# Optimization experiments

Measured on AMD Instinct MI355X. Metric: run time of the kernel, lower is better.

## Reference

```python
import jax, jax.numpy as jnp
import numpy as np

NUM_HEADS = 4
EPS = 1e-5


def conv1(W, b, z):
    # Conv1d with kernel_size=1 == channel-wise linear: (B, Cin, L) -> (B, Cout, L)
    return jnp.einsum('oi,bil->bol', W, z) + b[None, :, None]


def setup_inputs() -> dict:
    key = jax.random.key(0)
    ks = jax.random.split(key, 16)
    B, D, N = 2, 256, 4096
    s = 0.05
    return {
        'x': jax.random.normal(ks[0], (B, D, N), jnp.float32),
        'source': jax.random.normal(ks[1], (B, D, N), jnp.float32),
        'Wq': jax.random.normal(ks[2], (D, D), jnp.float32) * s,
        'bq': jax.random.normal(ks[3], (D,), jnp.float32) * s,
        'Wk': jax.random.normal(ks[4], (D, D), jnp.float32) * s,
        'bk': jax.random.normal(ks[5], (D,), jnp.float32) * s,
        'Wv': jax.random.normal(ks[6], (D, D), jnp.float32) * s,
        'bv': jax.random.normal(ks[7], (D,), jnp.float32) * s,
        'Wm': jax.random.normal(ks[8], (D, D), jnp.float32) * s,
        'bm': jax.random.normal(ks[9], (D,), jnp.float32) * s,
        'W1': jax.random.normal(ks[10], (2 * D, 2 * D), jnp.float32) * s,
        'b1': jax.random.normal(ks[11], (2 * D,), jnp.float32) * s,
        'W2': jax.random.normal(ks[12], (D, 2 * D), jnp.float32) * s,
        'b2': jax.random.normal(ks[13], (D,), jnp.float32) * s,
    }


def reference(x, source, Wq, bq, Wk, bk, Wv, bv, Wm, bm, W1, b1, W2, b2):
    B, D, N = x.shape
    M = source.shape[2]
    H = NUM_HEADS
    dim = D // H  # per-head dim; torch reshape splits channels as (dim, heads)

    q = conv1(Wq, bq, x).reshape(B, dim, H, N)
    k = conv1(Wk, bk, source).reshape(B, dim, H, M)
    v = conv1(Wv, bv, source).reshape(B, dim, H, M)

    scores = jnp.einsum('bdhn,bdhm->bhnm', q, k) / (dim ** 0.5)
    prob = jax.nn.softmax(scores, axis=-1)
    attn = jnp.einsum('bhnm,bdhm->bdhn', prob, v).reshape(B, D, N)

    message = conv1(Wm, bm, attn)

    h = conv1(W1, b1, jnp.concatenate([x, message], axis=1))
    # InstanceNorm1d (affine=False, biased var over L)
    mu = jnp.mean(h, axis=2, keepdims=True)
    var = jnp.mean((h - mu) ** 2, axis=2, keepdims=True)
    h = jax.nn.relu((h - mu) / jnp.sqrt(var + EPS))
    return conv1(W2, b2, h)
```

## Files before the change

### kernel.cpp

```cpp
#include <hip/hip_runtime.h>
#include <cstdint>
#include <cstddef>


typedef __attribute__((ext_vector_type(8))) short short8;
typedef __attribute__((ext_vector_type(4))) float floatx4;

union U4 { unsigned int u[4]; short8 s; };

__device__ __forceinline__ unsigned short f2bf(float x) {
  union { float f; unsigned int u; } c; c.f = x;
  unsigned int r = c.u + 0x7FFFu + ((c.u >> 16) & 1u);
  return (unsigned short)(r >> 16);
}
__device__ __forceinline__ float bf2f(unsigned short u) {
  union { unsigned int i; float f; } c; c.i = ((unsigned int)u) << 16; return c.f;
}
__device__ __forceinline__ void gload16(const void* g, void* l) {
  __builtin_amdgcn_global_load_lds(
      (const __attribute__((address_space(1))) unsigned int*)g,
      (__attribute__((address_space(3))) unsigned int*)l, 16, 0, 0);
}
__device__ __forceinline__ unsigned int cvtpk(float lo, float hi) {
  unsigned int r;
  asm("v_cvt_pk_bf16_f32 %0, %1, %2" : "=v"(r) : "v"(lo), "v"(hi));
  return r;
}

#define LOG2E_8 0.18033688011112042f

__global__ __launch_bounds__(256) void tx_all(
    const float* __restrict__ x, const float* __restrict__ src,
    unsigned short* __restrict__ xb, unsigned short* __restrict__ sb,
    int C, int N)
{
  __shared__ float tile[32][33];
  const int which = blockIdx.z >> 1, b = blockIdx.z & 1;
  const float* X = which ? src : x;
  unsigned short* Y = which ? sb : xb;
  const int n0 = blockIdx.x * 32, c0 = blockIdx.y * 32;
  const int tc = threadIdx.x & 31, tr = threadIdx.x >> 5;
  #pragma unroll
  for (int i = 0; i < 4; ++i)
    tile[tr + i * 8][tc] = X[((size_t)b * C + c0 + tr + i * 8) * N + n0 + tc];
  __syncthreads();
  #pragma unroll
  for (int i = 0; i < 4; ++i)
    Y[((size_t)b * N + n0 + tr + i * 8) * C + c0 + tc] = f2bf(tile[tc][tr + i * 8]);
}

__global__ __launch_bounds__(256) void wprep(
    const float* __restrict__ Wq, const float* __restrict__ Wk,
    const float* __restrict__ Wv, const float* __restrict__ Wm,
    const float* __restrict__ W1, const float* __restrict__ W2,
    const float* __restrict__ bq, const float* __restrict__ bk,
    const float* __restrict__ bv, const float* __restrict__ bm,
    const float* __restrict__ b1, const float* __restrict__ b2,
    unsigned short* __restrict__ wqkv, unsigned short* __restrict__ wm_,
    unsigned short* __restrict__ w1_, unsigned short* __restrict__ w2_,
    float* __restrict__ biasb)
{
  const int bid = blockIdx.x, t = threadIdx.x;
  if (bid < 768) {
    const int idx = bid * 256 + t;
    const int op = idx >> 8, ip = idx & 255;
    const int grp = op >> 8, oo = op & 255;
    const int o = 4 * (oo & 63) + (oo >> 6);
    const float* W = grp == 0 ? Wq : grp == 1 ? Wk : Wv;
    const float sc = grp == 0 ? LOG2E_8 : 1.f;
    wqkv[idx] = f2bf(W[(size_t)o * 256 + ip] * sc);
  } else if (bid < 1024) {
    const int idx = (bid - 768) * 256 + t;
    const int op = idx >> 8, ip = idx & 255;
    const int i2 = 4 * (ip & 63) + (ip >> 6);
    wm_[idx] = f2bf(Wm[(size_t)op * 256 + i2]);
  } else if (bid < 2048) {
    const int idx = (bid - 1024) * 256 + t;
    w1_[idx] = f2bf(W1[idx]);
  } else if (bid < 2560) {
    const int idx = (bid - 2048) * 256 + t;
    w2_[idx] = f2bf(W2[idx]);
  } else {
    const int z = (bid - 2560) * 256 + t;
    if (z < 256)       biasb[z] = bq[4 * (z & 63) + (z >> 6)] * LOG2E_8;
    else if (z < 512)  { const int y = z - 256; biasb[z] = bk[4 * (y & 63) + (y >> 6)]; }
    else if (z < 768)  { const int y = z - 512; biasb[z] = bv[4 * (y & 63) + (y >> 6)]; }
    else if (z < 1024) biasb[z] = bm[z - 768];
    else if (z < 1536) biasb[z] = b1[z - 1024];
    else if (z < 1792) biasb[z] = b2[z - 1536];
  }
}

__global__ __launch_bounds__(256) void gemm128(
    const unsigned short* __restrict__ Wb, const float* __restrict__ bias,
    const unsigned short* __restrict__ X0, const unsigned short* __restrict__ X1,
    void* __restrict__ O0, void* __restrict__ O1, void* __restrict__ O2,
    int Co, int Ci, int Ci0, int N, int variant)
{
  const int n0 = blockIdx.x * 128;
  const int o0 = blockIdx.y * 128;
  const int b  = blockIdx.z;
  const int t  = threadIdx.x;
  const int w = t >> 6, lane = t & 63, qd = lane >> 4, l = lane & 15;
  const int oh = (w >> 1) * 64, nh = (w & 1) * 64;

  __shared__ unsigned short Wl[128 * 64];
  __shared__ unsigned short Xl[128 * 64];

  floatx4 acc[4][4];
  #pragma unroll
  for (int i = 0; i < 4; ++i)
    #pragma unroll
    for (int j = 0; j < 4; ++j) acc[i][j] = (floatx4){0.f, 0.f, 0.f, 0.f};

  for (int k0 = 0; k0 < Ci; k0 += 64) {
    const unsigned short* Xs; int cb, rl;
    if (variant == 1) { Xs = (o0 < 256) ? X0 : X1; cb = k0; rl = Ci; }
    else if (k0 < Ci0) { Xs = X0; cb = k0; rl = Ci0; }
    else               { Xs = X1; cb = k0 - Ci0; rl = Ci - Ci0; }
    __syncthreads();
    #pragma unroll
    for (int i = 0; i < 4; ++i) {
      const int idx = i * 256 + t;
      const int row = idx >> 3, pg = idx & 7, sg = pg ^ (row & 7);
      gload16(&Wb[(size_t)(o0 + row) * Ci + k0 + sg * 8], &Wl[row * 64 + pg * 8]);
      gload16(&Xs[((size_t)b * N + n0 + row) * rl + cb + sg * 8], &Xl[row * 64 + pg * 8]);
    }
    __syncthreads();

    short8 af[4][2], bf[4][2];
    #pragma unroll
    for (int i = 0; i < 4; ++i) {
      const int ar = oh + 16 * i + l;
      af[i][0] = *(const short8*)&Wl[ar * 64 + ((qd ^ (ar & 7))) * 8];
      af[i][1] = *(const short8*)&Wl[ar * 64 + (((4 + qd) ^ (ar & 7))) * 8];
    }
    #pragma unroll
    for (int j = 0; j < 4; ++j) {
      const int br = nh + 16 * j + l;
      bf[j][0] = *(const short8*)&Xl[br * 64 + ((qd ^ (br & 7))) * 8];
      bf[j][1] = *(const short8*)&Xl[br * 64 + (((4 + qd) ^ (br & 7))) * 8];
    }
    #pragma unroll
    for (int i = 0; i < 4; ++i)
      #pragma unroll
      for (int j = 0; j < 4; ++j) {
        acc[i][j] = __builtin_amdgcn_mfma_f32_16x16x32_bf16(af[i][0], bf[j][0], acc[i][j], 0, 0, 0);
        acc[i][j] = __builtin_amdgcn_mfma_f32_16x16x32_bf16(af[i][1], bf[j][1], acc[i][j], 0, 0, 0);
      }
  }

  const int osec = o0 + oh;
  #pragma unroll
  for (int i = 0; i < 4; ++i) {
    const int o4 = o0 + oh + 16 * i + qd * 4;
    const float4 bi = *(const float4*)&bias[o4];
    #pragma unroll
    for (int j = 0; j < 4; ++j) {
      const int n = n0 + nh + 16 * j + l;
      if (variant == 0) {
        unsigned short* C = (unsigned short*)O0;
        ushort4 pk;
        pk.x = f2bf(acc[i][j][0] + bi.x); pk.y = f2bf(acc[i][j][1] + bi.y);
        pk.z = f2bf(acc[i][j][2] + bi.z); pk.w = f2bf(acc[i][j][3] + bi.w);
        *(ushort4*)&C[((size_t)b * N + n) * Co + o4] = pk;
      } else if (variant == 1) {
        if (osec < 256) {
          unsigned short* C = (unsigned short*)O0;
          ushort4 pk;
          pk.x = f2bf(acc[i][j][0] + bi.x); pk.y = f2bf(acc[i][j][1] + bi.y);
          pk.z = f2bf(acc[i][j][2] + bi.z); pk.w = f2bf(acc[i][j][3] + bi.w);
          *(ushort4*)&C[((size_t)b * N + n) * 256 + o4] = pk;
        } else if (osec < 512) {
          unsigned short* C = (unsigned short*)O1;
          ushort4 pk;
          pk.x = f2bf(acc[i][j][0] + bi.x); pk.y = f2bf(acc[i][j][1] + bi.y);
          pk.z = f2bf(acc[i][j][2] + bi.z); pk.w = f2bf(acc[i][j][3] + bi.w);
          *(ushort4*)&C[((size_t)b * N + n) * 256 + (o4 - 256)] = pk;
        } else {
          unsigned short* C = (unsigned short*)O2;
          #pragma unroll
          for (int rg = 0; rg < 4; ++rg) {
            const int op = o4 - 512 + rg, h = op >> 6, d = op & 63;
            C[(((size_t)b * 4 + h) * 64 + d) * N + n] =
                f2bf(acc[i][j][rg] + ((const float*)&bi)[rg]);
          }
        }
      } else {
        float* C = (float*)O0;
        #pragma unroll
        for (int rg = 0; rg < 4; ++rg)
          C[((size_t)b * Co + o4 + rg) * N + n] = acc[i][j][rg] + ((const float*)&bi)[rg];
      }
    }
  }
}

__global__ __launch_bounds__(256) void attn_mfma(
    const unsigned short* __restrict__ qb, const unsigned short* __restrict__ kb,
    const unsigned short* __restrict__ vh, unsigned short* __restrict__ Opart,
    float* __restrict__ liPart, int N)
{
  const int qt = blockIdx.x;
  const int h  = blockIdx.y;
  const int b  = blockIdx.z >> 2, s = blockIdx.z & 3;
  const int n0 = qt * 128;
  const int t  = threadIdx.x;
  const int w = t >> 6, lane = t & 63, qd = lane >> 4, l = lane & 15;

  __shared__ unsigned short Kl[2][64 * 64];
  __shared__ unsigned short Vl[2][64 * 64];

  const unsigned short* qp0 = &qb[((size_t)b * N + n0 + 16 * w + l) * 256 + h * 64];
  const unsigned short* qp1 = qp0 + (size_t)64 * 256;
  short8 bQ[2][2];
  bQ[0][0] = *(const short8*)&qp0[qd * 8];
  bQ[0][1] = *(const short8*)&qp0[32 + qd * 8];
  bQ[1][0] = *(const short8*)&qp1[qd * 8];
  bQ[1][1] = *(const short8*)&qp1[32 + qd * 8];

  short8 ones;
  #pragma unroll
  for (int i = 0; i < 8; ++i) ones[i] = (short)0x3F80;

  floatx4 accO[2][4];
  floatx4 accLi[2];
  #pragma unroll
  for (int qs = 0; qs < 2; ++qs) {
    accLi[qs] = (floatx4){0.f, 0.f, 0.f, 0.f};
    #pragma unroll
    for (int ds = 0; ds < 4; ++ds) accO[qs][ds] = (floatx4){0.f, 0.f, 0.f, 0.f};
  }

  const int j0base = s * 1024;

  auto STAGE = [&](int buf, int j0) {
    #pragma unroll
    for (int i = 0; i < 2; ++i) {
      const int idx = i * 256 + t;
      const int row = idx >> 3, pg = idx & 7, sg = pg ^ (row & 7);
      gload16(&kb[((size_t)b * N + j0 + row) * 256 + h * 64 + sg * 8],
              &Kl[buf][row * 64 + pg * 8]);
      gload16(&vh[(((size_t)b * 4 + h) * 64 + row) * N + j0 + sg * 8],
              &Vl[buf][row * 64 + pg * 8]);
    }
  };

  STAGE(0, j0base);

  #pragma unroll 2
  for (int jt = 0; jt < 16; ++jt) {
    const int cur = jt & 1;
    __syncthreads();
    if (jt < 15) STAGE(cur ^ 1, j0base + (jt + 1) * 64);

    floatx4 S[2][4];
    __builtin_amdgcn_s_setprio(1);
    #pragma unroll
    for (int js = 0; js < 4; ++js) {
      const int br = 16 * js + l;
      const short8 k0 = *(const short8*)&Kl[cur][br * 64 + ((qd ^ (br & 7))) * 8];
      const short8 k1 = *(const short8*)&Kl[cur][br * 64 + (((4 + qd) ^ (br & 7))) * 8];
      floatx4 a0 = (floatx4){0.f, 0.f, 0.f, 0.f};
      floatx4 a1 = (floatx4){0.f, 0.f, 0.f, 0.f};
      a0 = __builtin_amdgcn_mfma_f32_16x16x32_bf16(k0, bQ[0][0], a0, 0, 0, 0);
      a1 = __builtin_amdgcn_mfma_f32_16x16x32_bf16(k0, bQ[1][0], a1, 0, 0, 0);
      a0 = __builtin_amdgcn_mfma_f32_16x16x32_bf16(k1, bQ[0][1], a0, 0, 0, 0);
      a1 = __builtin_amdgcn_mfma_f32_16x16x32_bf16(k1, bQ[1][1], a1, 0, 0, 0);
      S[0][js] = a0; S[1][js] = a1;
    }
    __builtin_amdgcn_s_setprio(0);

    unsigned int T[2][2][4];
    #pragma unroll
    for (int qs = 0; qs < 2; ++qs) {
      unsigned int U[4], W[4];
      #pragma unroll
      for (int js = 0; js < 4; ++js) {
        const float p0 = __builtin_exp2f(S[qs][js][0]);
        const float p1 = __builtin_exp2f(S[qs][js][1]);
        const float p2 = __builtin_exp2f(S[qs][js][2]);
        const float p3 = __builtin_exp2f(S[qs][js][3]);
        U[js] = cvtpk(p0, p1);
        W[js] = cvtpk(p2, p3);
      }
      #pragma unroll
      for (int js2 = 0; js2 < 2; ++js2) {
        unsigned int t0 = U[2 * js2], t2 = U[2 * js2 + 1];
        asm("v_permlane32_swap_b32 %0, %1" : "+v"(t0), "+v"(t2));
        asm("v_permlane16_swap_b32 %0, %1" : "+v"(t0), "+v"(t2));
        unsigned int t1 = W[2 * js2], t3 = W[2 * js2 + 1];
        asm("v_permlane32_swap_b32 %0, %1" : "+v"(t1), "+v"(t3));
        asm("v_permlane16_swap_b32 %0, %1" : "+v"(t1), "+v"(t3));
        T[qs][js2][0] = t0; T[qs][js2][1] = t1;
        T[qs][js2][2] = t2; T[qs][js2][3] = t3;
      }
    }

    __builtin_amdgcn_s_setprio(1);
    #pragma unroll
    for (int js2 = 0; js2 < 2; ++js2) {
      short8 vv[4];
      #pragma unroll
      for (int ds = 0; ds < 4; ++ds) {
        const int vr = 16 * ds + l;
        vv[ds] = *(const short8*)&Vl[cur][vr * 64 + (((4 * js2 + qd) ^ (vr & 7))) * 8];
      }
      #pragma unroll
      for (int qs = 0; qs < 2; ++qs) {
        U4 pu;
        pu.u[0] = T[qs][js2][0]; pu.u[1] = T[qs][js2][1];
        pu.u[2] = T[qs][js2][2]; pu.u[3] = T[qs][js2][3];
        const short8 pa = pu.s;
        #pragma unroll
        for (int ds = 0; ds < 4; ++ds)
          accO[qs][ds] = __builtin_amdgcn_mfma_f32_16x16x32_bf16(pa, vv[ds], accO[qs][ds], 0, 0, 0);
        accLi[qs] = __builtin_amdgcn_mfma_f32_16x16x32_bf16(pa, ones, accLi[qs], 0, 0, 0);
      }
    }
    __builtin_amdgcn_s_setprio(0);
  }

  const size_t obase = ((((size_t)b * 4 + h) * 4 + s) * 32 + qt) * 128;
  #pragma unroll
  for (int qs = 0; qs < 2; ++qs)
    #pragma unroll
    for (int rg = 0; rg < 4; ++rg) {
      const int q = qs * 64 + 16 * w + qd * 4 + rg;
      #pragma unroll
      for (int ds = 0; ds < 4; ++ds)
        Opart[(obase + q) * 64 + 16 * ds + l] = f2bf(accO[qs][ds][rg]);
      if (l == 0) liPart[obase + q] = accLi[qs][rg];
    }
}

__global__ __launch_bounds__(256) void attn_combine(
    const unsigned short* __restrict__ Opart, const float* __restrict__ liPart,
    unsigned short* __restrict__ atb, int N)
{
  const int qt = blockIdx.x, h = blockIdx.y, b = blockIdx.z;
  const int t = threadIdx.x;
  const int q = t >> 1, d0 = (t & 1) * 32;

  float li = 0.f;
  size_t idx[4];
  #pragma unroll
  for (int s = 0; s < 4; ++s) {
    idx[s] = ((((size_t)b * 4 + h) * 4 + s) * 32 + qt) * 128 + q;
    li += liPart[idx[s]];
  }
  const float inv = 1.f / li;

  float o[32];
  #pragma unroll
  for (int c = 0; c < 32; ++c) o[c] = 0.f;
  #pragma unroll
  for (int s = 0; s < 4; ++s) {
    #pragma unroll
    for (int c4 = 0; c4 < 4; ++c4) {
      const short8 v = *(const short8*)&Opart[idx[s] * 64 + d0 + c4 * 8];
      #pragma unroll
      for (int j = 0; j < 8; ++j) o[c4 * 8 + j] += bf2f((unsigned short)v[j]);
    }
  }
  unsigned short* dst = &atb[((size_t)b * N + qt * 128 + q) * 256 + h * 64 + d0];
  #pragma unroll
  for (int c4 = 0; c4 < 4; ++c4) {
    ushort4 pk;
    pk.x = f2bf(o[c4 * 8 + 0] * inv); pk.y = f2bf(o[c4 * 8 + 1] * inv);
    pk.z = f2bf(o[c4 * 8 + 2] * inv); pk.w = f2bf(o[c4 * 8 + 3] * inv);
    *(ushort4*)&dst[c4 * 8] = pk;
    pk.x = f2bf(o[c4 * 8 + 4] * inv); pk.y = f2bf(o[c4 * 8 + 5] * inv);
    pk.z = f2bf(o[c4 * 8 + 6] * inv); pk.w = f2bf(o[c4 * 8 + 7] * inv);
    *(ushort4*)&dst[c4 * 8 + 4] = pk;
  }
}

__global__ __launch_bounds__(256) void in_stats(
    const unsigned short* __restrict__ H, float* __restrict__ Ps,
    float* __restrict__ Ps2, int N)
{
  const int cg = blockIdx.x, ns = blockIdx.y, b = blockIdx.z, t = threadIdx.x;
  const int c0 = cg * 64 + (t & 7) * 8;
  float s[8] = {}, s2[8] = {};
  #pragma unroll
  for (int i = 0; i < 8; ++i) {
    const int n = ns * 256 + (t >> 3) + i * 32;
    const short8 hv = *(const short8*)&H[((size_t)b * N + n) * 512 + c0];
    #pragma unroll
    for (int j = 0; j < 8; ++j) {
      const float f = bf2f((unsigned short)hv[j]);
      s[j] += f; s2[j] += f * f;
    }
  }
  __shared__ float rs[32][64], rs2[32][64];
  #pragma unroll
  for (int j = 0; j < 8; ++j) {
    rs[t >> 3][(t & 7) * 8 + j] = s[j];
    rs2[t >> 3][(t & 7) * 8 + j] = s2[j];
  }
  __syncthreads();
  if (t < 64) {
    float a = 0.f, a2 = 0.f;
    #pragma unroll
    for (int r = 0; r < 32; ++r) { a += rs[r][t]; a2 += rs2[r][t]; }
    const size_t o = ((size_t)ns * 2 + b) * 512 + cg * 64 + t;
    Ps[o] = a; Ps2[o] = a2;
  }
}

__global__ __launch_bounds__(256) void in_norm(
    unsigned short* __restrict__ H, const float* __restrict__ Ps,
    const float* __restrict__ Ps2, int N)
{
  const int cg = blockIdx.x, ns = blockIdx.y, b = blockIdx.z, t = threadIdx.x;
  __shared__ float muS[64], ivS[64];
  if (t < 64) {
    const int c = cg * 64 + t;
    float s = 0.f, s2 = 0.f;
    for (int k = 0; k < 16; ++k) {
      s  += Ps [((size_t)k * 2 + b) * 512 + c];
      s2 += Ps2[((size_t)k * 2 + b) * 512 + c];
    }
    const float mu = s / (float)N;
    const float var = fmaxf(s2 / (float)N - mu * mu, 0.f);
    muS[t] = mu;
    ivS[t] = rsqrtf(var + 1e-5f);
  }
  __syncthreads();
  const int c0 = cg * 64 + (t & 7) * 8;
  float mu[8], iv[8];
  #pragma unroll
  for (int j = 0; j < 8; ++j) {
    mu[j] = muS[(t & 7) * 8 + j];
    iv[j] = ivS[(t & 7) * 8 + j];
  }
  #pragma unroll
  for (int i = 0; i < 8; ++i) {
    const int n = ns * 256 + (t >> 3) + i * 32;
    unsigned short* p = &H[((size_t)b * N + n) * 512 + c0];
    short8 hv = *(const short8*)p;
    #pragma unroll
    for (int j = 0; j < 8; ++j) {
      const float f = fmaxf((bf2f((unsigned short)hv[j]) - mu[j]) * iv[j], 0.f);
      hv[j] = (short)f2bf(f);
    }
    *(short8*)p = hv;
  }
}

extern "C" void kernel_launch(void* const* d_in, const int* in_sizes, int n_in,
                              void* d_out, int out_size, void* d_ws, size_t ws_size,
                              hipStream_t stream)
{
  const int B = 2, D = 256, N = 4096;

  const float* x   = (const float*)d_in[0];
  const float* src = (const float*)d_in[1];
  const float* Wq  = (const float*)d_in[2];  const float* bq = (const float*)d_in[3];
  const float* Wk  = (const float*)d_in[4];  const float* bk = (const float*)d_in[5];
  const float* Wv  = (const float*)d_in[6];  const float* bv = (const float*)d_in[7];
  const float* Wm  = (const float*)d_in[8];  const float* bm = (const float*)d_in[9];
  const float* W1  = (const float*)d_in[10]; const float* b1 = (const float*)d_in[11];
  const float* W2  = (const float*)d_in[12]; const float* b2 = (const float*)d_in[13];
  float* out = (float*)d_out;

  char* ws = (char*)d_ws;
  const size_t MB = 1u << 20;
  unsigned short* xb  = (unsigned short*)(ws + 0 * MB);
  unsigned short* sb  = (unsigned short*)(ws + 4 * MB);
  unsigned short* qbf = (unsigned short*)(ws + 8 * MB);
  unsigned short* kbf = (unsigned short*)(ws + 12 * MB);
  unsigned short* vhb = (unsigned short*)(ws + 16 * MB);
  unsigned short* atb = (unsigned short*)(ws + 20 * MB);
  unsigned short* Opart = (unsigned short*)(ws + 24 * MB);
  unsigned short* msb = (unsigned short*)(ws + 24 * MB);
  unsigned short* hb  = (unsigned short*)(ws + 28 * MB);
  float* liPart = (float*)(ws + 41 * MB);
  unsigned short* wqkvb = (unsigned short*)(ws + 42 * MB);
  unsigned short* wmb = wqkvb + 768 * 256;
  unsigned short* w1b = wmb + 256 * 256;
  unsigned short* w2b = w1b + 512 * 512;
  float* biasb = (float*)(ws + 44 * MB);
  float* Ps    = biasb + 2048;
  float* Ps2   = Ps + 16 * 2 * 512;

  const dim3 blk(256);

  tx_all<<<dim3(N / 32, D / 32, 2 * B), blk, 0, stream>>>(x, src, xb, sb, D, N);
  wprep<<<dim3(2567), blk, 0, stream>>>(Wq, Wk, Wv, Wm, W1, W2,
                                        bq, bk, bv, bm, b1, b2,
                                        wqkvb, wmb, w1b, w2b, biasb);

  gemm128<<<dim3(N / 128, 6, B), blk, 0, stream>>>(
      wqkvb, biasb, xb, sb, qbf, kbf, vhb, 768, 256, 256, N, 1);

  attn_mfma<<<dim3(N / 128, 4, B * 4), blk, 0, stream>>>(
      qbf, kbf, vhb, Opart, liPart, N);
  attn_combine<<<dim3(N / 128, 4, B), blk, 0, stream>>>(Opart, liPart, atb, N);

  gemm128<<<dim3(N / 128, 2, B), blk, 0, stream>>>(
      wmb, biasb + 768, atb, atb, msb, nullptr, nullptr, 256, 256, 256, N, 0);

  gemm128<<<dim3(N / 128, 4, B), blk, 0, stream>>>(
      w1b, biasb + 1024, xb, msb, hb, nullptr, nullptr, 512, 512, 256, N, 0);

  in_stats<<<dim3(8, 16, B), blk, 0, stream>>>(hb, Ps, Ps2, N);
  in_norm<<<dim3(8, 16, B), blk, 0, stream>>>(hb, Ps, Ps2, N);

  gemm128<<<dim3(N / 128, 2, B), blk, 0, stream>>>(
      w2b, biasb + 1536, hb, hb, out, nullptr, nullptr, 256, 512, 512, N, 2);
}
```

Baseline: 220.2 us.

## Double-buffer GEMM LDS tiles and merge input/weight prep kernels

The two preprocessing launches (activation transpose-to-bf16 and weight/bias conversion) are merged into one kernel, with the block index choosing the role. The GEMM moves to two LDS buffers, issuing the next K-slice's global-to-LDS loads before computing on the current one, with one barrier per iteration. The goal is to hide load latency behind MFMA work and save a launch. It doubles LDS use per block to 64KB, which may cut occupancy, and the single barrier leaves the buffer-reuse ordering fragile.

```diff
diff --git a/kernel.cpp b/kernel.cpp
--- a/kernel.cpp
+++ b/kernel.cpp
@@ -29,27 +29,9 @@
 
 #define LOG2E_8 0.18033688011112042f
 
-__global__ __launch_bounds__(256) void tx_all(
+__global__ __launch_bounds__(256) void prep_all(
     const float* __restrict__ x, const float* __restrict__ src,
     unsigned short* __restrict__ xb, unsigned short* __restrict__ sb,
-    int C, int N)
-{
-  __shared__ float tile[32][33];
-  const int which = blockIdx.z >> 1, b = blockIdx.z & 1;
-  const float* X = which ? src : x;
-  unsigned short* Y = which ? sb : xb;
-  const int n0 = blockIdx.x * 32, c0 = blockIdx.y * 32;
-  const int tc = threadIdx.x & 31, tr = threadIdx.x >> 5;
-  #pragma unroll
-  for (int i = 0; i < 4; ++i)
-    tile[tr + i * 8][tc] = X[((size_t)b * C + c0 + tr + i * 8) * N + n0 + tc];
-  __syncthreads();
-  #pragma unroll
-  for (int i = 0; i < 4; ++i)
-    Y[((size_t)b * N + n0 + tr + i * 8) * C + c0 + tc] = f2bf(tile[tc][tr + i * 8]);
-}
-
-__global__ __launch_bounds__(256) void wprep(
     const float* __restrict__ Wq, const float* __restrict__ Wk,
     const float* __restrict__ Wv, const float* __restrict__ Wm,
     const float* __restrict__ W1, const float* __restrict__ W2,
@@ -58,9 +40,29 @@
     const float* __restrict__ b1, const float* __restrict__ b2,
     unsigned short* __restrict__ wqkv, unsigned short* __restrict__ wm_,
     unsigned short* __restrict__ w1_, unsigned short* __restrict__ w2_,
-    float* __restrict__ biasb)
-{
-  const int bid = blockIdx.x, t = threadIdx.x;
+    float* __restrict__ biasb, int C, int N)
+{
+  const int t = threadIdx.x;
+  if (blockIdx.x < 4096) {
+    __shared__ float tile[32][33];
+    const int tb = blockIdx.x;
+    const int z = tb >> 10, rem = tb & 1023;
+    const int bx = rem & 127, by = rem >> 7;
+    const int which = z >> 1, b = z & 1;
+    const float* X = which ? src : x;
+    unsigned short* Y = which ? sb : xb;
+    const int n0 = bx * 32, c0 = by * 32;
+    const int tc = t & 31, tr = t >> 5;
+    #pragma unroll
+    for (int i = 0; i < 4; ++i)
+      tile[tr + i * 8][tc] = X[((size_t)b * C + c0 + tr + i * 8) * N + n0 + tc];
+    __syncthreads();
+    #pragma unroll
+    for (int i = 0; i < 4; ++i)
+      Y[((size_t)b * N + n0 + tr + i * 8) * C + c0 + tc] = f2bf(tile[tc][tr + i * 8]);
+    return;
+  }
+  const int bid = blockIdx.x - 4096;
   if (bid < 768) {
     const int idx = bid * 256 + t;
     const int op = idx >> 8, ip = idx & 255;
@@ -104,8 +106,8 @@
   const int w = t >> 6, lane = t & 63, qd = lane >> 4, l = lane & 15;
   const int oh = (w >> 1) * 64, nh = (w & 1) * 64;
 
-  __shared__ unsigned short Wl[128 * 64];
-  __shared__ unsigned short Xl[128 * 64];
+  __shared__ unsigned short Wl[2][128 * 64];
+  __shared__ unsigned short Xl[2][128 * 64];
 
   floatx4 acc[4][4];
   #pragma unroll
@@ -113,33 +115,40 @@
     #pragma unroll
     for (int j = 0; j < 4; ++j) acc[i][j] = (floatx4){0.f, 0.f, 0.f, 0.f};
 
-  for (int k0 = 0; k0 < Ci; k0 += 64) {
+  auto STAGE = [&](int buf, int k0) {
     const unsigned short* Xs; int cb, rl;
     if (variant == 1) { Xs = (o0 < 256) ? X0 : X1; cb = k0; rl = Ci; }
     else if (k0 < Ci0) { Xs = X0; cb = k0; rl = Ci0; }
     else               { Xs = X1; cb = k0 - Ci0; rl = Ci - Ci0; }
-    __syncthreads();
     #pragma unroll
     for (int i = 0; i < 4; ++i) {
       const int idx = i * 256 + t;
       const int row = idx >> 3, pg = idx & 7, sg = pg ^ (row & 7);
-      gload16(&Wb[(size_t)(o0 + row) * Ci + k0 + sg * 8], &Wl[row * 64 + pg * 8]);
-      gload16(&Xs[((size_t)b * N + n0 + row) * rl + cb + sg * 8], &Xl[row * 64 + pg * 8]);
-    }
+      gload16(&Wb[(size_t)(o0 + row) * Ci + k0 + sg * 8], &Wl[buf][row * 64 + pg * 8]);
+      gload16(&Xs[((size_t)b * N + n0 + row) * rl + cb + sg * 8], &Xl[buf][row * 64 + pg * 8]);
+    }
+  };
+
+  STAGE(0, 0);
+  const int nk = Ci >> 6;
+  #pragma unroll 2
+  for (int ks = 0; ks < nk; ++ks) {
+    const int cur = ks & 1;
     __syncthreads();
+    if (ks + 1 < nk) STAGE(cur ^ 1, (ks + 1) * 64);
 
     short8 af[4][2], bf[4][2];
     #pragma unroll
     for (int i = 0; i < 4; ++i) {
       const int ar = oh + 16 * i + l;
-      af[i][0] = *(const short8*)&Wl[ar * 64 + ((qd ^ (ar & 7))) * 8];
-      af[i][1] = *(const short8*)&Wl[ar * 64 + (((4 + qd) ^ (ar & 7))) * 8];
+      af[i][0] = *(const short8*)&Wl[cur][ar * 64 + ((qd ^ (ar & 7))) * 8];
+      af[i][1] = *(const short8*)&Wl[cur][ar * 64 + (((4 + qd) ^ (ar & 7))) * 8];
     }
     #pragma unroll
     for (int j = 0; j < 4; ++j) {
       const int br = nh + 16 * j + l;
-      bf[j][0] = *(const short8*)&Xl[br * 64 + ((qd ^ (br & 7))) * 8];
-      bf[j][1] = *(const short8*)&Xl[br * 64 + (((4 + qd) ^ (br & 7))) * 8];
+      bf[j][0] = *(const short8*)&Xl[cur][br * 64 + ((qd ^ (br & 7))) * 8];
+      bf[j][1] = *(const short8*)&Xl[cur][br * 64 + (((4 + qd) ^ (br & 7))) * 8];
     }
     #pragma unroll
     for (int i = 0; i < 4; ++i)
@@ -487,10 +496,9 @@
 
   const dim3 blk(256);
 
-  tx_all<<<dim3(N / 32, D / 32, 2 * B), blk, 0, stream>>>(x, src, xb, sb, D, N);
-  wprep<<<dim3(2567), blk, 0, stream>>>(Wq, Wk, Wv, Wm, W1, W2,
-                                        bq, bk, bv, bm, b1, b2,
-                                        wqkvb, wmb, w1b, w2b, biasb);
+  prep_all<<<dim3(4096 + 2567), blk, 0, stream>>>(
+      x, src, xb, sb, Wq, Wk, Wv, Wm, W1, W2,
+      bq, bk, bv, bm, b1, b2, wqkvb, wmb, w1b, w2b, biasb, D, N);
 
   gemm128<<<dim3(N / 128, 6, B), blk, 0, stream>>>(
       wqkvb, biasb, xb, sb, qbf, kbf, vhb, 768, 256, 256, N, 1);
```

New measurement: 227.3 us. 3.2% more time.

## Fold message projection into W1 and merge prep kernels

Applied to the files above, without the earlier changes.

Precomputes the product of W1's second half with Wm as a small GEMM, and folds bm into b1, so the message conv is no longer run over the full sequence. The first FFN GEMM now reads the attention output directly using a split weight (W1a for x, the combined weight for attn). The input transpose and weight-prep kernels are merged into one launch to cut launch overhead. This adds a tiny weight GEMM and a serial per-output bias dot product in the prep kernel, and rounds the combined weight to bf16, which changes numerics slightly.

```diff
diff --git a/kernel.cpp b/kernel.cpp
--- a/kernel.cpp
+++ b/kernel.cpp
@@ -29,38 +29,41 @@
 
 #define LOG2E_8 0.18033688011112042f
 
-__global__ __launch_bounds__(256) void tx_all(
+__global__ __launch_bounds__(256) void prep_all(
     const float* __restrict__ x, const float* __restrict__ src,
     unsigned short* __restrict__ xb, unsigned short* __restrict__ sb,
-    int C, int N)
-{
-  __shared__ float tile[32][33];
-  const int which = blockIdx.z >> 1, b = blockIdx.z & 1;
-  const float* X = which ? src : x;
-  unsigned short* Y = which ? sb : xb;
-  const int n0 = blockIdx.x * 32, c0 = blockIdx.y * 32;
-  const int tc = threadIdx.x & 31, tr = threadIdx.x >> 5;
-  #pragma unroll
-  for (int i = 0; i < 4; ++i)
-    tile[tr + i * 8][tc] = X[((size_t)b * C + c0 + tr + i * 8) * N + n0 + tc];
-  __syncthreads();
-  #pragma unroll
-  for (int i = 0; i < 4; ++i)
-    Y[((size_t)b * N + n0 + tr + i * 8) * C + c0 + tc] = f2bf(tile[tc][tr + i * 8]);
-}
-
-__global__ __launch_bounds__(256) void wprep(
     const float* __restrict__ Wq, const float* __restrict__ Wk,
     const float* __restrict__ Wv, const float* __restrict__ Wm,
     const float* __restrict__ W1, const float* __restrict__ W2,
     const float* __restrict__ bq, const float* __restrict__ bk,
     const float* __restrict__ bv, const float* __restrict__ bm,
     const float* __restrict__ b1, const float* __restrict__ b2,
-    unsigned short* __restrict__ wqkv, unsigned short* __restrict__ wm_,
-    unsigned short* __restrict__ w1_, unsigned short* __restrict__ w2_,
-    float* __restrict__ biasb)
-{
-  const int bid = blockIdx.x, t = threadIdx.x;
+    unsigned short* __restrict__ wqkv, unsigned short* __restrict__ wmT,
+    unsigned short* __restrict__ w1a, unsigned short* __restrict__ w1bb,
+    unsigned short* __restrict__ w2_, float* __restrict__ biasb,
+    float* __restrict__ bcb, int C, int N)
+{
+  const int t = threadIdx.x;
+  if (blockIdx.x < 4096) {
+    __shared__ float tile[32][33];
+    const int tb = blockIdx.x;
+    const int z = tb >> 10, rem = tb & 1023;
+    const int bx = rem & 127, by = rem >> 7;
+    const int which = z >> 1, b = z & 1;
+    const float* X = which ? src : x;
+    unsigned short* Y = which ? sb : xb;
+    const int n0 = bx * 32, c0 = by * 32;
+    const int tc = t & 31, tr = t >> 5;
+    #pragma unroll
+    for (int i = 0; i < 4; ++i)
+      tile[tr + i * 8][tc] = X[((size_t)b * C + c0 + tr + i * 8) * N + n0 + tc];
+    __syncthreads();
+    #pragma unroll
+    for (int i = 0; i < 4; ++i)
+      Y[((size_t)b * N + n0 + tr + i * 8) * C + c0 + tc] = f2bf(tile[tc][tr + i * 8]);
+    return;
+  }
+  const int bid = blockIdx.x - 4096;
   if (bid < 768) {
     const int idx = bid * 256 + t;
     const int op = idx >> 8, ip = idx & 255;
@@ -71,31 +74,42 @@
     wqkv[idx] = f2bf(W[(size_t)o * 256 + ip] * sc);
   } else if (bid < 1024) {
     const int idx = (bid - 768) * 256 + t;
-    const int op = idx >> 8, ip = idx & 255;
-    const int i2 = 4 * (ip & 63) + (ip >> 6);
-    wm_[idx] = f2bf(Wm[(size_t)op * 256 + i2]);
+    const int hm = idx >> 8, c = idx & 255;
+    const int ph = 4 * (hm & 63) + (hm >> 6);
+    wmT[idx] = f2bf(Wm[(size_t)c * 256 + ph]);
+  } else if (bid < 1536) {
+    const int idx = (bid - 1024) * 256 + t;
+    const int o = idx >> 8, c = idx & 255;
+    w1a[idx] = f2bf(W1[(size_t)o * 512 + c]);
   } else if (bid < 2048) {
-    const int idx = (bid - 1024) * 256 + t;
-    w1_[idx] = f2bf(W1[idx]);
+    const int idx = (bid - 1536) * 256 + t;
+    const int o = idx >> 8, c = idx & 255;
+    w1bb[idx] = f2bf(W1[(size_t)o * 512 + 256 + c]);
   } else if (bid < 2560) {
     const int idx = (bid - 2048) * 256 + t;
     w2_[idx] = f2bf(W2[idx]);
-  } else {
+  } else if (bid < 2566) {
     const int z = (bid - 2560) * 256 + t;
     if (z < 256)       biasb[z] = bq[4 * (z & 63) + (z >> 6)] * LOG2E_8;
     else if (z < 512)  { const int y = z - 256; biasb[z] = bk[4 * (y & 63) + (y >> 6)]; }
     else if (z < 768)  { const int y = z - 512; biasb[z] = bv[4 * (y & 63) + (y >> 6)]; }
-    else if (z < 1024) biasb[z] = bm[z - 768];
-    else if (z < 1536) biasb[z] = b1[z - 1024];
-    else if (z < 1792) biasb[z] = b2[z - 1536];
+    else if (z < 1280) biasb[z] = 0.f;
+    else if (z < 1536) biasb[z] = b2[z - 1280];
+  } else {
+    const int o = (bid - 2566) * 256 + t;
+    float a = b1[o];
+    for (int c = 0; c < 256; ++c)
+      a += W1[(size_t)o * 512 + 256 + c] * bm[c];
+    bcb[o] = a;
   }
 }
 
 __global__ __launch_bounds__(256) void gemm128(
-    const unsigned short* __restrict__ Wb, const float* __restrict__ bias,
+    const unsigned short* __restrict__ W0, const unsigned short* __restrict__ W1p,
+    const float* __restrict__ bias,
     const unsigned short* __restrict__ X0, const unsigned short* __restrict__ X1,
     void* __restrict__ O0, void* __restrict__ O1, void* __restrict__ O2,
-    int Co, int Ci, int Ci0, int N, int variant)
+    int Co, int Ci, int Ci0, int Wci0, int N, int variant)
 {
   const int n0 = blockIdx.x * 128;
   const int o0 = blockIdx.y * 128;
@@ -118,12 +132,15 @@
     if (variant == 1) { Xs = (o0 < 256) ? X0 : X1; cb = k0; rl = Ci; }
     else if (k0 < Ci0) { Xs = X0; cb = k0; rl = Ci0; }
     else               { Xs = X1; cb = k0 - Ci0; rl = Ci - Ci0; }
+    const unsigned short* Ws; int wb, wrl;
+    if (k0 < Wci0) { Ws = W0; wb = k0; wrl = Wci0; }
+    else           { Ws = W1p; wb = k0 - Wci0; wrl = Ci - Wci0; }
     __syncthreads();
     #pragma unroll
     for (int i = 0; i < 4; ++i) {
       const int idx = i * 256 + t;
       const int row = idx >> 3, pg = idx & 7, sg = pg ^ (row & 7);
-      gload16(&Wb[(size_t)(o0 + row) * Ci + k0 + sg * 8], &Wl[row * 64 + pg * 8]);
+      gload16(&Ws[(size_t)(o0 + row) * wrl + wb + sg * 8], &Wl[row * 64 + pg * 8]);
       gload16(&Xs[((size_t)b * N + n0 + row) * rl + cb + sg * 8], &Xl[row * 64 + pg * 8]);
     }
     __syncthreads();
@@ -186,11 +203,16 @@
                 f2bf(acc[i][j][rg] + ((const float*)&bi)[rg]);
           }
         }
-      } else {
+      } else if (variant == 2) {
         float* C = (float*)O0;
         #pragma unroll
         for (int rg = 0; rg < 4; ++rg)
           C[((size_t)b * Co + o4 + rg) * N + n] = acc[i][j][rg] + ((const float*)&bi)[rg];
+      } else {
+        unsigned short* C = (unsigned short*)O0;
+        #pragma unroll
+        for (int rg = 0; rg < 4; ++rg)
+          C[(size_t)(o4 + rg) * N + n] = f2bf(acc[i][j][rg] + ((const float*)&bi)[rg]);
       }
     }
   }
@@ -474,40 +496,42 @@
   unsigned short* vhb = (unsigned short*)(ws + 16 * MB);
   unsigned short* atb = (unsigned short*)(ws + 20 * MB);
   unsigned short* Opart = (unsigned short*)(ws + 24 * MB);
-  unsigned short* msb = (unsigned short*)(ws + 24 * MB);
   unsigned short* hb  = (unsigned short*)(ws + 28 * MB);
   float* liPart = (float*)(ws + 41 * MB);
   unsigned short* wqkvb = (unsigned short*)(ws + 42 * MB);
-  unsigned short* wmb = wqkvb + 768 * 256;
-  unsigned short* w1b = wmb + 256 * 256;
-  unsigned short* w2b = w1b + 512 * 512;
+  unsigned short* wmT  = wqkvb + 768 * 256;
+  unsigned short* w1a  = wmT + 256 * 256;
+  unsigned short* w1bb = w1a + 512 * 256;
+  unsigned short* w2b  = w1bb + 512 * 256;
+  unsigned short* wcb  = w2b + 256 * 512;
   float* biasb = (float*)(ws + 44 * MB);
+  float* bcb   = biasb + 1536;
   float* Ps    = biasb + 2048;
   float* Ps2   = Ps + 16 * 2 * 512;
 
   const dim3 blk(256);
 
-  tx_all<<<dim3(N / 32, D / 32, 2 * B), blk, 0, stream>>>(x, src, xb, sb, D, N);
-  wprep<<<dim3(2567), blk, 0, stream>>>(Wq, Wk, Wv, Wm, W1, W2,
-                                        bq, bk, bv, bm, b1, b2,
-                                        wqkvb, wmb, w1b, w2b, biasb);
+  prep_all<<<dim3(4096 + 2568), blk, 0, stream>>>(
+      x, src, xb, sb, Wq, Wk, Wv, Wm, W1, W2,
+      bq, bk, bv, bm, b1, b2, wqkvb, wmT, w1a, w1bb, w2b, biasb, bcb, D, N);
+
+  gemm128<<<dim3(2, 4, 1), blk, 0, stream>>>(
+      w1bb, w1bb, biasb + 768 , wmT, wmT,
+      wcb, nullptr, nullptr, 512, 256, 256, 256, 256, 3);
 
   gemm128<<<dim3(N / 128, 6, B), blk, 0, stream>>>(
-      wqkvb, biasb, xb, sb, qbf, kbf, vhb, 768, 256, 256, N, 1);
+      wqkvb, wqkvb, biasb, xb, sb, qbf, kbf, vhb, 768, 256, 256, 256, N, 1);
 
   attn_mfma<<<dim3(N / 128, 4, B * 4), blk, 0, stream>>>(
       qbf, kbf, vhb, Opart, liPart, N);
   attn_combine<<<dim3(N / 128, 4, B), blk, 0, stream>>>(Opart, liPart, atb, N);
 
-  gemm128<<<dim3(N / 128, 2, B), blk, 0, stream>>>(
-      wmb, biasb + 768, atb, atb, msb, nullptr, nullptr, 256, 256, 256, N, 0);
-
   gemm128<<<dim3(N / 128, 4, B), blk, 0, stream>>>(
-      w1b, biasb + 1024, xb, msb, hb, nullptr, nullptr, 512, 512, 256, N, 0);
+      w1a, wcb, bcb, xb, atb, hb, nullptr, nullptr, 512, 512, 256, 256, N, 0);
 
   in_stats<<<dim3(8, 16, B), blk, 0, stream>>>(hb, Ps, Ps2, N);
   in_norm<<<dim3(8, 16, B), blk, 0, stream>>>(hb, Ps, Ps2, N);
 
   gemm128<<<dim3(N / 128, 2, B), blk, 0, stream>>>(
-      w2b, biasb + 1536, hb, hb, out, nullptr, nullptr, 256, 512, 512, N, 2);
-}
+      w2b, w2b, biasb + 1280, hb, hb, out, nullptr, nullptr, 256, 512, 512, 512, N, 2);
+}
```

After: 226.3 us. 1.03x slower.
